# Optimization experiments

Measured on AMD Instinct MI355X. Metric: run time of the kernel, lower is better.

The kernel has to match this reference:

```python
import jax, jax.numpy as jnp
import numpy as np

DIM = 256
HEADS = 8
HEAD_DIM = DIM // HEADS          # 32 (v head dim, also defines scale)
QK_DIM = DIM // HEADS // 2       # 16 (q/k head dim)
SCALE = HEAD_DIM ** -0.5


def conv3x3(x, w, b):
    # x: [B,C,H,W], w: [O,I,3,3] (torch OIHW), padding=1 stride=1 == SAME
    y = jax.lax.conv_general_dilated(
        x, w, window_strides=(1, 1), padding='SAME',
        dimension_numbers=('NCHW', 'OIHW', 'NCHW'))
    return y + b[None, :, None, None]


def setup_inputs() -> dict:
    key = jax.random.key(0)
    ks = jax.random.split(key, 12)
    s = 0.02
    B, C, H, W = 1, DIM, 64, 64
    return {
        'x':       jax.random.normal(ks[0], (B, C, H, W), jnp.float32),
        'attn_kv': jax.random.normal(ks[1], (B, C, H, W), jnp.float32),
        'qw':  jax.random.normal(ks[2], (C, C, 3, 3), jnp.float32) * s,
        'qb':  jnp.zeros((C,), jnp.float32),
        'kvw': jax.random.normal(ks[3], (C, C, 3, 3), jnp.float32) * s,
        'kvb': jnp.zeros((C,), jnp.float32),
        'Wq':  jax.random.normal(ks[4], (C // 2, C), jnp.float32) * s,
        'bq':  jnp.zeros((C // 2,), jnp.float32),
        'Wk':  jax.random.normal(ks[5], (C // 2, C), jnp.float32) * s,
        'bk':  jnp.zeros((C // 2,), jnp.float32),
        'Wv':  jax.random.normal(ks[6], (C, C), jnp.float32) * s,
        'bv':  jnp.zeros((C,), jnp.float32),
        'Wp':  jax.random.normal(ks[7], (C, C), jnp.float32) * s,
        'bp':  jnp.zeros((C,), jnp.float32),
    }


def reference(x, attn_kv, qw, qb, kvw, kvb, Wq, bq, Wk, bk, Wv, bv, Wp, bp):
    B, C, Hh, Ww = x.shape
    N = Hh * Ww
    # conv projections
    xq = conv3x3(x, qw, qb)            # [B,C,H,W]
    kv = conv3x3(attn_kv, kvw, kvb)    # [B,C,H,W]
    # flatten to tokens [B,N,C]
    xf = xq.reshape(B, C, N).transpose(0, 2, 1)
    kvf = kv.reshape(B, C, N).transpose(0, 2, 1)
    # qkv projections with asymmetric head dims
    q = (xf @ Wq.T + bq).reshape(B, N, HEADS, QK_DIM).transpose(0, 2, 1, 3)    # [B,h,N,16]
    k = (kvf @ Wk.T + bk).reshape(B, N, HEADS, QK_DIM).transpose(0, 2, 1, 3)   # [B,h,N,16]
    v = (kvf @ Wv.T + bv).reshape(B, N, HEADS, HEAD_DIM).transpose(0, 2, 1, 3) # [B,h,N,32]
    # attention (manual softmax(q k^T) v)
    attn = jax.nn.softmax(jnp.einsum('bhnd,bhmd->bhnm', q * SCALE, k), axis=-1)  # [B,h,N,N]
    o = jnp.einsum('bhnm,bhmd->bhnd', attn, v)  # [B,h,N,32]
    # replicate the original transpose(1,2).reshape(B,N,C) on the [1,B,h,N,dv]
    # tensor: memory order becomes (h, B, N, dv) flattened into (B, N, C).
    o = jnp.transpose(o, (1, 0, 2, 3)).reshape(B, N, C)
    out = o @ Wp.T + bp                               # [B,N,C]
    return out.transpose(0, 2, 1).reshape(B, C, Hh, Ww)
```

## Files before the change

kernel.cpp:

```cpp
#include <hip/hip_runtime.h>

typedef unsigned short u16;
typedef __attribute__((ext_vector_type(8))) short bf16x8;
typedef __attribute__((ext_vector_type(4))) float f32x4;
typedef __attribute__((ext_vector_type(16))) float f32x16;
typedef __attribute__((ext_vector_type(4))) unsigned u32x4;
typedef __attribute__((ext_vector_type(2))) int i32x2;

struct alignas(8) u16x4 { u16 x, y, z, w; };

#define MFMA16(A, B, C) __builtin_amdgcn_mfma_f32_16x16x32_bf16(A, B, C, 0, 0, 0)
#define MFMA32(A, B, C) __builtin_amdgcn_mfma_f32_32x32x16_bf16(A, B, C, 0, 0, 0)
#define QSCALE (0.17677669529663689f * 1.4426950408889634f)

__device__ __forceinline__ u16 f2bf(float f) {
  unsigned u = __float_as_uint(f);
  u = (u + 0x7fffu + ((u >> 16) & 1u)) >> 16;
  return (u16)u;
}

__device__ __forceinline__ bf16x8 ldb8(const u16* p) {
  return *reinterpret_cast<const bf16x8*>(p);
}

__device__ __forceinline__ void glds16(const u16* g, u16* l) {
  __builtin_amdgcn_global_load_lds(
      (const __attribute__((address_space(1))) void*)g,
      (__attribute__((address_space(3))) void*)l, 16, 0, 0);
}

__global__ __launch_bounds__(256) void prep_kernel(
    const float* __restrict__ x, const float* __restrict__ akv,
    const float* __restrict__ qw, const float* __restrict__ kvw,
    const float* __restrict__ Wq, const float* __restrict__ Wk,
    const float* __restrict__ Wv, const float* __restrict__ Wp,
    u16* __restrict__ xpT, u16* __restrict__ w2,
    u16* __restrict__ wqs, u16* __restrict__ wks,
    u16* __restrict__ wvs, u16* __restrict__ wps)
{
  __shared__ float sm[64 * 65];
  const int b = blockIdx.x, t = threadIdx.x;
  if (b < 512) {
    const int z = b >> 8, rem = b & 255;
    const int cib = (rem >> 6) * 64, y = rem & 63;
    const float* in = (z ? akv : x);
    const int tc = t & 63, tr = t >> 6;
    #pragma unroll
    for (int i = 0; i < 16; ++i) {
      const int ci = i * 4 + tr;
      sm[ci * 65 + tc] = in[(size_t)(cib + ci) * 4096 + y * 64 + tc];
    }
    __syncthreads();
    u16* dst = xpT + (size_t)z * 4356 * 256;
    #pragma unroll
    for (int i = 0; i < 16; ++i) {
      const int px = i * 4 + tr;
      dst[(size_t)((y + 1) * 66 + px + 1) * 256 + cib + tc] = f2bf(sm[tc * 65 + px]);
    }
    return;
  }
  if (b < 642) {
    const int slot = (b - 512) * 4 + (t >> 6);
    const int z = slot >= 260 ? 1 : 0;
    const int j = slot - z * 260;
    int pos;
    if (j < 66) pos = j;
    else if (j < 132) pos = 65 * 66 + (j - 66);
    else { const int j2 = j - 132; pos = (1 + (j2 >> 1)) * 66 + (j2 & 1) * 65; }
    u16x4 zr = {0, 0, 0, 0};
    *reinterpret_cast<u16x4*>(xpT + (size_t)z * 4356 * 256 + (size_t)pos * 256 + (t & 63) * 4) = zr;
    return;
  }
  if (b < 1154) {
    const int idx = b - 642;
    const int z = idx >> 8, co = idx & 255;
    const float* src = (z ? kvw : qw) + (size_t)co * 2304;
    u16* dst = w2 + (size_t)z * 256 * 2304 + (size_t)co * 2304;
    #pragma unroll
    for (int i = 0; i < 9; ++i) sm[i * 256 + t] = src[i * 256 + t];
    __syncthreads();
    #pragma unroll
    for (int i = 0; i < 9; ++i) dst[i * 256 + t] = f2bf(sm[t * 9 + i]);
    return;
  }
  {
    int idx = (b - 1154) * 256 + t;
    if (idx < 32768) { wqs[idx] = f2bf(Wq[idx] * QSCALE); return; }
    idx -= 32768;
    if (idx < 32768) { wks[idx] = f2bf(Wk[idx]); return; }
    idx -= 32768;
    if (idx < 65536) { wvs[idx] = f2bf(Wv[idx]); return; }
    idx -= 65536;
    wps[idx] = f2bf(Wp[idx]);
  }
}

__global__ __launch_bounds__(256, 2) void conv_kernel(
    const u16* __restrict__ xpT, const u16* __restrict__ w2,
    const float* __restrict__ qb, const float* __restrict__ kvb,
    u16* __restrict__ xqt, u16* __restrict__ kvt)
{
  __shared__ u16 ab[3][64 * 64];
  __shared__ u16 bb[3][64 * 64];

  const int z = blockIdx.z;
  const u16* __restrict__ X = xpT + (size_t)z * 4356 * 256;
  const u16* __restrict__ W = w2 + (size_t)z * 256 * 2304;
  const float* bias = z ? kvb : qb;
  u16* out = z ? kvt : xqt;

  const int lane = threadIdx.x & 63, w = threadIdx.x >> 6;
  const int lo = lane & 15, g = lane >> 4;
  const int r8 = lane >> 3, c = lane & 7;
  const int wr = w >> 1, wc = w & 1;
  const int cobase = blockIdx.x * 64;
  const int tbase = blockIdx.y * 64;

  const bool isA = (w < 2);
  const u16* gb[4];
  int ldso[4];
  #pragma unroll
  for (int q = 0; q < 4; ++q) {
    const int flat = w * 4 + q;
    if (flat < 8) {
      const int j = flat;
      gb[q] = W + (size_t)(cobase + j * 8 + r8) * 2304 + (c ^ r8) * 8;
      ldso[q] = j * 512;
    } else {
      const int j = flat - 8;
      const int tok = tbase + j * 8 + r8;
      const int padrow = ((tok >> 6) + 1) * 66 + (tok & 63) + 1;
      gb[q] = X + (size_t)padrow * 256 + (c ^ r8) * 8;
      ldso[q] = j * 512;
    }
  }

  f32x4 acc[2][2] = {};

  auto stage = [&](int s, int bsel) {
    int srcoff;
    if (isA) {
      srcoff = s * 64;
    } else {
      const int kk = s >> 2;
      const int koff = (kk / 3 - 1) * 66 + (kk % 3) - 1;
      srcoff = koff * 256 + (s & 3) * 64;
    }
    u16* lb = isA ? ab[bsel] : bb[bsel];
    #pragma unroll
    for (int q = 0; q < 4; ++q)
      glds16(gb[q] + srcoff, lb + ldso[q]);
  };

  stage(0, 0);
  stage(1, 1);
  asm volatile("s_waitcnt vmcnt(4)" ::: "memory");
  __syncthreads();

  #pragma unroll 1
  for (int s = 0; s < 36; ++s) {
    const int cur = s % 3;
    if (s + 2 < 36) stage(s + 2, (s + 2) % 3);
    #pragma unroll
    for (int ks = 0; ks < 2; ++ks) {
      const int swz = ((ks * 4 + g) ^ (lo & 7)) * 8;
      const int rowA = wr * 32 + lo, colB = wc * 32 + lo;
      bf16x8 a0 = *reinterpret_cast<const bf16x8*>(&ab[cur][rowA * 64 + swz]);
      bf16x8 a1 = *reinterpret_cast<const bf16x8*>(&ab[cur][(rowA + 16) * 64 + swz]);
      bf16x8 b0 = *reinterpret_cast<const bf16x8*>(&bb[cur][colB * 64 + swz]);
      bf16x8 b1 = *reinterpret_cast<const bf16x8*>(&bb[cur][(colB + 16) * 64 + swz]);
      acc[0][0] = MFMA16(a0, b0, acc[0][0]);
      acc[0][1] = MFMA16(a0, b1, acc[0][1]);
      acc[1][0] = MFMA16(a1, b0, acc[1][0]);
      acc[1][1] = MFMA16(a1, b1, acc[1][1]);
    }
    if (s < 35) {
      if (s + 2 < 36) asm volatile("s_waitcnt vmcnt(4)" ::: "memory");
      else            asm volatile("s_waitcnt vmcnt(0)" ::: "memory");
      __syncthreads();
    }
  }

  #pragma unroll
  for (int af = 0; af < 2; ++af) {
    const int cb = cobase + wr * 32 + af * 16 + 4 * g;
    const float4 bi = *reinterpret_cast<const float4*>(bias + cb);
    #pragma unroll
    for (int bf = 0; bf < 2; ++bf) {
      const int t = tbase + wc * 32 + bf * 16 + lo;
      f32x4 v = acc[af][bf];
      u16x4 pk = { f2bf(v[0] + bi.x), f2bf(v[1] + bi.y),
                   f2bf(v[2] + bi.z), f2bf(v[3] + bi.w) };
      *reinterpret_cast<u16x4*>(out + (size_t)t * 256 + cb) = pk;
    }
  }
}

__global__ __launch_bounds__(256) void qkv_kernel(
    const u16* __restrict__ xqt, const u16* __restrict__ kvt,
    const u16* __restrict__ wqs, const u16* __restrict__ wks,
    const u16* __restrict__ wvs,
    const float* __restrict__ bq, const float* __restrict__ bk,
    const float* __restrict__ bv,
    u16* __restrict__ Qh, u16* __restrict__ Kh, u16* __restrict__ Vp)
{
  const int lane = threadIdx.x & 63, wid = threadIdx.x >> 6;
  const int lo = lane & 15, g = lane >> 4;
  const int bx = blockIdx.x;

  if (blockIdx.z == 0) {
    const bool isq = bx < 2;
    const u16* A = isq ? wqs : wks;
    const u16* Bm = isq ? xqt : kvt;
    const float* bias = isq ? bq : bk;
    const float bsc = isq ? (float)QSCALE : 1.f;
    u16* outp = isq ? Qh : Kh;
    const int c0 = (bx & 1) * 64 + (wid >> 1) * 32;
    const int n0 = blockIdx.y * 64 + (wid & 1) * 32;

    f32x4 acc[2][2] = {};
    #pragma unroll
    for (int s = 0; s < 8; ++s) {
      const int k0 = s * 32 + 8 * g;
      bf16x8 A0 = ldb8(A + (c0 + lo) * 256 + k0);
      bf16x8 A1 = ldb8(A + (c0 + 16 + lo) * 256 + k0);
      bf16x8 B0 = ldb8(Bm + (n0 + lo) * 256 + k0);
      bf16x8 B1 = ldb8(Bm + (n0 + 16 + lo) * 256 + k0);
      acc[0][0] = MFMA16(A0, B0, acc[0][0]);
      acc[0][1] = MFMA16(A0, B1, acc[0][1]);
      acc[1][0] = MFMA16(A1, B0, acc[1][0]);
      acc[1][1] = MFMA16(A1, B1, acc[1][1]);
    }
    #pragma unroll
    for (int af = 0; af < 2; ++af) {
      const int cb = c0 + af * 16 + 4 * g;
      const int h = cb >> 4, dd = cb & 15;
      const float4 bi = *reinterpret_cast<const float4*>(bias + cb);
      #pragma unroll
      for (int bfr = 0; bfr < 2; ++bfr) {
        const int n = n0 + bfr * 16 + lo;
        f32x4 v = acc[af][bfr];
        u16x4 pk = { f2bf(v[0] + bi.x * bsc), f2bf(v[1] + bi.y * bsc),
                     f2bf(v[2] + bi.z * bsc), f2bf(v[3] + bi.w * bsc) };
        *reinterpret_cast<u16x4*>(outp + h * 65536 + n * 16 + dd) = pk;
      }
    }
  } else {
    const int n0 = blockIdx.y * 64 + (wid >> 1) * 32;
    const int c0 = bx * 64 + (wid & 1) * 32;

    f32x4 acc[2][2] = {};
    #pragma unroll
    for (int s = 0; s < 8; ++s) {
      const int k0 = s * 32 + 8 * g;
      bf16x8 A0 = ldb8(kvt + (n0 + lo) * 256 + k0);
      bf16x8 A1 = ldb8(kvt + (n0 + 16 + lo) * 256 + k0);
      bf16x8 B0 = ldb8(wvs + (c0 + lo) * 256 + k0);
      bf16x8 B1 = ldb8(wvs + (c0 + 16 + lo) * 256 + k0);
      acc[0][0] = MFMA16(A0, B0, acc[0][0]);
      acc[0][1] = MFMA16(A0, B1, acc[0][1]);
      acc[1][0] = MFMA16(A1, B0, acc[1][0]);
      acc[1][1] = MFMA16(A1, B1, acc[1][1]);
    }
    #pragma unroll
    for (int af = 0; af < 2; ++af) {
      const int nb = n0 + af * 16 + 4 * g;
      const int tblk = nb >> 4, hhalf = (nb >> 3) & 1, j0 = nb & 7;
      #pragma unroll
      for (int bfr = 0; bfr < 2; ++bfr) {
        const int cc = c0 + bfr * 16 + lo;
        const int h = cc >> 5, dv = cc & 31;
        const float bi = bv[cc];
        f32x4 v = acc[af][bfr];
        u16x4 pk = { f2bf(v[0] + bi), f2bf(v[1] + bi),
                     f2bf(v[2] + bi), f2bf(v[3] + bi) };
        *reinterpret_cast<u16x4*>(
            Vp + (size_t)h * 131072 + tblk * 512 + hhalf * 256 + dv * 8 + j0) = pk;
      }
    }
  }
}

__global__ __launch_bounds__(512, 4) void attn_kernel(
    const u16* __restrict__ Qh, const u16* __restrict__ Kh,
    const u16* __restrict__ Vp, u16* __restrict__ O2)
{
  __shared__ float olds[16][8][64];
  __shared__ float l_ldsA[8][32], l_ldsB[8][32];
  __shared__ float invA[32], invB[32];

  const int lane = threadIdx.x & 63, w = threadIdx.x >> 6;
  const int lo = lane & 31, hi = lane >> 5;
  const int bx = blockIdx.x;
  const int h = bx & 7, qg = bx >> 3;
  const int qt0 = qg * 64;

  const u16* Q = Qh + h * 65536;
  const u16* K = Kh + h * 65536;

  const bf16x8 qbA = ldb8(Q + (qt0 + lo) * 16 + 8 * hi);
  const bf16x8 qbB = ldb8(Q + (qt0 + 32 + lo) * 16 + 8 * hi);

  f32x16 oA = {0,0,0,0,0,0,0,0,0,0,0,0,0,0,0,0};
  f32x16 oB = {0,0,0,0,0,0,0,0,0,0,0,0,0,0,0,0};
  float lA0 = 0.f, lA1 = 0.f, lB0 = 0.f, lB1 = 0.f;
  const int kvbase = w * 512;

  const u16* kptr = K + (kvbase + lo) * 16 + 8 * hi;
  const u16* vptr = Vp + (size_t)h * 131072 + (size_t)kvbase * 32 + lane * 8;

  #pragma unroll 1
  for (int st = 0; st < 16; ++st) {
    const bf16x8 kb = ldb8(kptr);
    const bf16x8 vb0 = ldb8(vptr);
    const bf16x8 vb1 = ldb8(vptr + 512);
    kptr += 512; vptr += 1024;

    const f32x16 zf = {0,0,0,0,0,0,0,0,0,0,0,0,0,0,0,0};

    {
      f32x16 s = MFMA32(kb, qbA, zf);
      unsigned cpk[8];
      #pragma unroll
      for (int r = 0; r < 16; r += 2) {
        const float p0 = __builtin_amdgcn_exp2f(s[r]);
        const float p1 = __builtin_amdgcn_exp2f(s[r + 1]);
        lA0 += p0; lA1 += p1;
        asm("v_cvt_pk_bf16_f32 %0, %1, %2" : "=v"(cpk[r >> 1]) : "v"(p0), "v"(p1));
      }
      u32x4 fa0, fa1;
      { i32x2 r2 = __builtin_amdgcn_permlane32_swap((int)cpk[0], (int)cpk[2], false, false);
        fa0[0] = (unsigned)r2[0]; fa0[2] = (unsigned)r2[1]; }
      { i32x2 r2 = __builtin_amdgcn_permlane32_swap((int)cpk[1], (int)cpk[3], false, false);
        fa0[1] = (unsigned)r2[0]; fa0[3] = (unsigned)r2[1]; }
      { i32x2 r2 = __builtin_amdgcn_permlane32_swap((int)cpk[4], (int)cpk[6], false, false);
        fa1[0] = (unsigned)r2[0]; fa1[2] = (unsigned)r2[1]; }
      { i32x2 r2 = __builtin_amdgcn_permlane32_swap((int)cpk[5], (int)cpk[7], false, false);
        fa1[1] = (unsigned)r2[0]; fa1[3] = (unsigned)r2[1]; }
      oA = MFMA32(__builtin_bit_cast(bf16x8, fa0), vb0, oA);
      oA = MFMA32(__builtin_bit_cast(bf16x8, fa1), vb1, oA);
    }
    {
      f32x16 s = MFMA32(kb, qbB, zf);
      unsigned cpk[8];
      #pragma unroll
      for (int r = 0; r < 16; r += 2) {
        const float p0 = __builtin_amdgcn_exp2f(s[r]);
        const float p1 = __builtin_amdgcn_exp2f(s[r + 1]);
        lB0 += p0; lB1 += p1;
        asm("v_cvt_pk_bf16_f32 %0, %1, %2" : "=v"(cpk[r >> 1]) : "v"(p0), "v"(p1));
      }
      u32x4 fa0, fa1;
      { i32x2 r2 = __builtin_amdgcn_permlane32_swap((int)cpk[0], (int)cpk[2], false, false);
        fa0[0] = (unsigned)r2[0]; fa0[2] = (unsigned)r2[1]; }
      { i32x2 r2 = __builtin_amdgcn_permlane32_swap((int)cpk[1], (int)cpk[3], false, false);
        fa0[1] = (unsigned)r2[0]; fa0[3] = (unsigned)r2[1]; }
      { i32x2 r2 = __builtin_amdgcn_permlane32_swap((int)cpk[4], (int)cpk[6], false, false);
        fa1[0] = (unsigned)r2[0]; fa1[2] = (unsigned)r2[1]; }
      { i32x2 r2 = __builtin_amdgcn_permlane32_swap((int)cpk[5], (int)cpk[7], false, false);
        fa1[1] = (unsigned)r2[0]; fa1[3] = (unsigned)r2[1]; }
      oB = MFMA32(__builtin_bit_cast(bf16x8, fa0), vb0, oB);
      oB = MFMA32(__builtin_bit_cast(bf16x8, fa1), vb1, oB);
    }
  }

  float lA = lA0 + lA1;  lA += __shfl_xor(lA, 32);
  float lB = lB0 + lB1;  lB += __shfl_xor(lB, 32);
  if (lane < 32) { l_ldsA[w][lane] = lA; l_ldsB[w][lane] = lB; }

  #pragma unroll
  for (int r = 0; r < 16; ++r) olds[r][w][lane] = oA[r];
  __syncthreads();

  if (w == 0 && lane < 32) {
    float L = 0.f;
    #pragma unroll
    for (int w2 = 0; w2 < 8; ++w2) L += l_ldsA[w2][lane];
    invA[lane] = 1.0f / L;
  }
  if (w == 1 && lane < 32) {
    float L = 0.f;
    #pragma unroll
    for (int w2 = 0; w2 < 8; ++w2) L += l_ldsB[w2][lane];
    invB[lane] = 1.0f / L;
  }
  __syncthreads();

  #pragma unroll
  for (int j = 0; j < 2; ++j) {
    const int r = 2 * w + j;
    const int q = (r & 3) + 8 * (r >> 2) + 4 * hi;
    float acc = 0.f;
    #pragma unroll
    for (int w2 = 0; w2 < 8; ++w2) acc += olds[r][w2][lane];
    acc *= invA[q];
    const int n = qt0 + q;
    O2[(size_t)((h << 9) + (n >> 3)) * 256 + ((n & 7) << 5) + lo] = f2bf(acc);
  }
  __syncthreads();

  #pragma unroll
  for (int r = 0; r < 16; ++r) olds[r][w][lane] = oB[r];
  __syncthreads();

  #pragma unroll
  for (int j = 0; j < 2; ++j) {
    const int r = 2 * w + j;
    const int q = (r & 3) + 8 * (r >> 2) + 4 * hi;
    float acc = 0.f;
    #pragma unroll
    for (int w2 = 0; w2 < 8; ++w2) acc += olds[r][w2][lane];
    acc *= invB[q];
    const int n = qt0 + 32 + q;
    O2[(size_t)((h << 9) + (n >> 3)) * 256 + ((n & 7) << 5) + lo] = f2bf(acc);
  }
}

__global__ __launch_bounds__(256) void oproj_kernel(
    const u16* __restrict__ O2, const u16* __restrict__ wps,
    const float* __restrict__ bp, float* __restrict__ outp)
{
  const int lane = threadIdx.x & 63, wid = threadIdx.x >> 6;
  const int lo = lane & 15, g = lane >> 4;
  const int n0 = blockIdx.x * 64 + (wid >> 1) * 32;
  const int c0 = blockIdx.y * 64 + (wid & 1) * 32;

  f32x4 acc[2][2] = {};
  #pragma unroll
  for (int s = 0; s < 8; ++s) {
    const int k0 = s * 32 + 8 * g;
    bf16x8 A0 = ldb8(O2 + (n0 + lo) * 256 + k0);
    bf16x8 A1 = ldb8(O2 + (n0 + 16 + lo) * 256 + k0);
    bf16x8 B0 = ldb8(wps + (c0 + lo) * 256 + k0);
    bf16x8 B1 = ldb8(wps + (c0 + 16 + lo) * 256 + k0);
    acc[0][0] = MFMA16(A0, B0, acc[0][0]);
    acc[0][1] = MFMA16(A0, B1, acc[0][1]);
    acc[1][0] = MFMA16(A1, B0, acc[1][0]);
    acc[1][1] = MFMA16(A1, B1, acc[1][1]);
  }
  #pragma unroll
  for (int af = 0; af < 2; ++af) {
    const int nb = n0 + af * 16 + 4 * g;
    #pragma unroll
    for (int bfr = 0; bfr < 2; ++bfr) {
      const int c = c0 + bfr * 16 + lo;
      const float bi = bp[c];
      f32x4 v = acc[af][bfr];
      float4 r4;
      r4.x = v[0] + bi; r4.y = v[1] + bi; r4.z = v[2] + bi; r4.w = v[3] + bi;
      *reinterpret_cast<float4*>(outp + (size_t)c * 4096 + nb) = r4;
    }
  }
}

extern "C" void kernel_launch(void* const* d_in, const int* in_sizes, int n_in,
                              void* d_out, int out_size, void* d_ws, size_t ws_size,
                              hipStream_t stream) {
  (void)in_sizes; (void)n_in; (void)out_size; (void)ws_size;
  const float* x   = (const float*)d_in[0];
  const float* akv = (const float*)d_in[1];
  const float* qw  = (const float*)d_in[2];
  const float* qb  = (const float*)d_in[3];
  const float* kvw = (const float*)d_in[4];
  const float* kvb = (const float*)d_in[5];
  const float* Wq  = (const float*)d_in[6];
  const float* bq  = (const float*)d_in[7];
  const float* Wk  = (const float*)d_in[8];
  const float* bk  = (const float*)d_in[9];
  const float* Wv  = (const float*)d_in[10];
  const float* bv  = (const float*)d_in[11];
  const float* Wp  = (const float*)d_in[12];
  const float* bp  = (const float*)d_in[13];
  float* outp = (float*)d_out;

  char* wsb = (char*)d_ws;
  size_t off = 0;
  auto take = [&](size_t bytes) {
    char* p = wsb + off;
    off = (off + bytes + 255) & ~(size_t)255;
    return p;
  };
  u16* xpT = (u16*)take(2ULL * 4356 * 256 * 2);
  u16* w2  = (u16*)take(2ULL * 256 * 2304 * 2);
  u16* wqs = (u16*)take(128ULL * 256 * 2);
  u16* wks = (u16*)take(128ULL * 256 * 2);
  u16* wvs = (u16*)take(256ULL * 256 * 2);
  u16* wps = (u16*)take(256ULL * 256 * 2);
  u16* xqt = (u16*)take(4096ULL * 256 * 2);
  u16* kvt = (u16*)take(4096ULL * 256 * 2);
  u16* Qh  = (u16*)take(8ULL * 4096 * 16 * 2);
  u16* Kh  = (u16*)take(8ULL * 4096 * 16 * 2);
  u16* Vp  = (u16*)take(8ULL * 131072 * 2);
  u16* O2  = (u16*)take(4096ULL * 256 * 2);

  prep_kernel<<<dim3(1922), dim3(256), 0, stream>>>(
      x, akv, qw, kvw, Wq, Wk, Wv, Wp, xpT, w2, wqs, wks, wvs, wps);
  conv_kernel<<<dim3(4, 64, 2), dim3(256), 0, stream>>>(xpT, w2, qb, kvb, xqt, kvt);
  qkv_kernel<<<dim3(4, 64, 2), dim3(256), 0, stream>>>(
      xqt, kvt, wqs, wks, wvs, bq, bk, bv, Qh, Kh, Vp);
  attn_kernel<<<dim3(512), dim3(512), 0, stream>>>(Qh, Kh, Vp, O2);
  oproj_kernel<<<dim3(64, 4), dim3(256), 0, stream>>>(O2, wps, bp, outp);
}
```

Baseline: 70.05 us.

## Software-prefetch operands in qkv/attn loops and shrink oproj tiles for more blocks

Adds register double-buffering to the qkv, attention and output-projection inner loops, loading the next K-step's operands before issuing the current MFMAs so global load latency overlaps with compute. The attention loop also issues both score MFMAs up front. The output projection is retiled from 32x32 per wave to 16x16 per wave with four times as many blocks, which raises parallelism but loses operand reuse. The extra live registers could reduce occupancy.

```diff
diff --git a/kernel.cpp b/kernel.cpp
--- a/kernel.cpp
+++ b/kernel.cpp
@@ -218,18 +218,26 @@
     const int c0 = (bx & 1) * 64 + (wid >> 1) * 32;
     const int n0 = blockIdx.y * 64 + (wid & 1) * 32;
 
+    const u16* Ar0 = A + (c0 + lo) * 256 + 8 * g;
+    const u16* Ar1 = A + (c0 + 16 + lo) * 256 + 8 * g;
+    const u16* Br0 = Bm + (n0 + lo) * 256 + 8 * g;
+    const u16* Br1 = Bm + (n0 + 16 + lo) * 256 + 8 * g;
+
     f32x4 acc[2][2] = {};
+    bf16x8 A0 = ldb8(Ar0), A1 = ldb8(Ar1), B0 = ldb8(Br0), B1 = ldb8(Br1);
     #pragma unroll
     for (int s = 0; s < 8; ++s) {
-      const int k0 = s * 32 + 8 * g;
-      bf16x8 A0 = ldb8(A + (c0 + lo) * 256 + k0);
-      bf16x8 A1 = ldb8(A + (c0 + 16 + lo) * 256 + k0);
-      bf16x8 B0 = ldb8(Bm + (n0 + lo) * 256 + k0);
-      bf16x8 B1 = ldb8(Bm + (n0 + 16 + lo) * 256 + k0);
+      bf16x8 A0n, A1n, B0n, B1n;
+      if (s < 7) {
+        const int kn = (s + 1) * 32;
+        A0n = ldb8(Ar0 + kn); A1n = ldb8(Ar1 + kn);
+        B0n = ldb8(Br0 + kn); B1n = ldb8(Br1 + kn);
+      }
       acc[0][0] = MFMA16(A0, B0, acc[0][0]);
       acc[0][1] = MFMA16(A0, B1, acc[0][1]);
       acc[1][0] = MFMA16(A1, B0, acc[1][0]);
       acc[1][1] = MFMA16(A1, B1, acc[1][1]);
+      A0 = A0n; A1 = A1n; B0 = B0n; B1 = B1n;
     }
     #pragma unroll
     for (int af = 0; af < 2; ++af) {
@@ -249,18 +257,26 @@
     const int n0 = blockIdx.y * 64 + (wid >> 1) * 32;
     const int c0 = bx * 64 + (wid & 1) * 32;
 
+    const u16* Ar0 = kvt + (n0 + lo) * 256 + 8 * g;
+    const u16* Ar1 = kvt + (n0 + 16 + lo) * 256 + 8 * g;
+    const u16* Br0 = wvs + (c0 + lo) * 256 + 8 * g;
+    const u16* Br1 = wvs + (c0 + 16 + lo) * 256 + 8 * g;
+
     f32x4 acc[2][2] = {};
+    bf16x8 A0 = ldb8(Ar0), A1 = ldb8(Ar1), B0 = ldb8(Br0), B1 = ldb8(Br1);
     #pragma unroll
     for (int s = 0; s < 8; ++s) {
-      const int k0 = s * 32 + 8 * g;
-      bf16x8 A0 = ldb8(kvt + (n0 + lo) * 256 + k0);
-      bf16x8 A1 = ldb8(kvt + (n0 + 16 + lo) * 256 + k0);
-      bf16x8 B0 = ldb8(wvs + (c0 + lo) * 256 + k0);
-      bf16x8 B1 = ldb8(wvs + (c0 + 16 + lo) * 256 + k0);
+      bf16x8 A0n, A1n, B0n, B1n;
+      if (s < 7) {
+        const int kn = (s + 1) * 32;
+        A0n = ldb8(Ar0 + kn); A1n = ldb8(Ar1 + kn);
+        B0n = ldb8(Br0 + kn); B1n = ldb8(Br1 + kn);
+      }
       acc[0][0] = MFMA16(A0, B0, acc[0][0]);
       acc[0][1] = MFMA16(A0, B1, acc[0][1]);
       acc[1][0] = MFMA16(A1, B0, acc[1][0]);
       acc[1][1] = MFMA16(A1, B1, acc[1][1]);
+      A0 = A0n; A1 = A1n; B0 = B0n; B1 = B1n;
     }
     #pragma unroll
     for (int af = 0; af < 2; ++af) {
@@ -309,22 +325,27 @@
   const u16* kptr = K + (kvbase + lo) * 16 + 8 * hi;
   const u16* vptr = Vp + (size_t)h * 131072 + (size_t)kvbase * 32 + lane * 8;
 
+  bf16x8 kb = ldb8(kptr);
+  bf16x8 vb0 = ldb8(vptr);
+  bf16x8 vb1 = ldb8(vptr + 512);
+
   #pragma unroll 1
   for (int st = 0; st < 16; ++st) {
-    const bf16x8 kb = ldb8(kptr);
-    const bf16x8 vb0 = ldb8(vptr);
-    const bf16x8 vb1 = ldb8(vptr + 512);
     kptr += 512; vptr += 1024;
+    const bf16x8 kb_n = ldb8(kptr);
+    const bf16x8 vb0_n = ldb8(vptr);
+    const bf16x8 vb1_n = ldb8(vptr + 512);
 
     const f32x16 zf = {0,0,0,0,0,0,0,0,0,0,0,0,0,0,0,0};
+    f32x16 sA = MFMA32(kb, qbA, zf);
+    f32x16 sB = MFMA32(kb, qbB, zf);
 
     {
-      f32x16 s = MFMA32(kb, qbA, zf);
       unsigned cpk[8];
       #pragma unroll
       for (int r = 0; r < 16; r += 2) {
-        const float p0 = __builtin_amdgcn_exp2f(s[r]);
-        const float p1 = __builtin_amdgcn_exp2f(s[r + 1]);
+        const float p0 = __builtin_amdgcn_exp2f(sA[r]);
+        const float p1 = __builtin_amdgcn_exp2f(sA[r + 1]);
         lA0 += p0; lA1 += p1;
         asm("v_cvt_pk_bf16_f32 %0, %1, %2" : "=v"(cpk[r >> 1]) : "v"(p0), "v"(p1));
       }
@@ -341,12 +362,11 @@
       oA = MFMA32(__builtin_bit_cast(bf16x8, fa1), vb1, oA);
     }
     {
-      f32x16 s = MFMA32(kb, qbB, zf);
       unsigned cpk[8];
       #pragma unroll
       for (int r = 0; r < 16; r += 2) {
-        const float p0 = __builtin_amdgcn_exp2f(s[r]);
-        const float p1 = __builtin_amdgcn_exp2f(s[r + 1]);
+        const float p0 = __builtin_amdgcn_exp2f(sB[r]);
+        const float p1 = __builtin_amdgcn_exp2f(sB[r + 1]);
         lB0 += p0; lB1 += p1;
         asm("v_cvt_pk_bf16_f32 %0, %1, %2" : "=v"(cpk[r >> 1]) : "v"(p0), "v"(p1));
       }
@@ -362,6 +382,7 @@
       oB = MFMA32(__builtin_bit_cast(bf16x8, fa0), vb0, oB);
       oB = MFMA32(__builtin_bit_cast(bf16x8, fa1), vb1, oB);
     }
+    kb = kb_n; vb0 = vb0_n; vb1 = vb1_n;
   }
 
   float lA = lA0 + lA1;  lA += __shfl_xor(lA, 32);
@@ -422,35 +443,29 @@
 {
   const int lane = threadIdx.x & 63, wid = threadIdx.x >> 6;
   const int lo = lane & 15, g = lane >> 4;
-  const int n0 = blockIdx.x * 64 + (wid >> 1) * 32;
-  const int c0 = blockIdx.y * 64 + (wid & 1) * 32;
-
-  f32x4 acc[2][2] = {};
+  const int n0 = blockIdx.x * 16;
+  const int c0 = blockIdx.y * 64 + wid * 16;
+
+  const u16* Ar = O2 + (n0 + lo) * 256 + 8 * g;
+  const u16* Br = wps + (c0 + lo) * 256 + 8 * g;
+
+  f32x4 acc = {};
+  bf16x8 A0 = ldb8(Ar), B0 = ldb8(Br);
   #pragma unroll
   for (int s = 0; s < 8; ++s) {
-    const int k0 = s * 32 + 8 * g;
-    bf16x8 A0 = ldb8(O2 + (n0 + lo) * 256 + k0);
-    bf16x8 A1 = ldb8(O2 + (n0 + 16 + lo) * 256 + k0);
-    bf16x8 B0 = ldb8(wps + (c0 + lo) * 256 + k0);
-    bf16x8 B1 = ldb8(wps + (c0 + 16 + lo) * 256 + k0);
-    acc[0][0] = MFMA16(A0, B0, acc[0][0]);
-    acc[0][1] = MFMA16(A0, B1, acc[0][1]);
-    acc[1][0] = MFMA16(A1, B0, acc[1][0]);
-    acc[1][1] = MFMA16(A1, B1, acc[1][1]);
-  }
-  #pragma unroll
-  for (int af = 0; af < 2; ++af) {
-    const int nb = n0 + af * 16 + 4 * g;
-    #pragma unroll
-    for (int bfr = 0; bfr < 2; ++bfr) {
-      const int c = c0 + bfr * 16 + lo;
-      const float bi = bp[c];
-      f32x4 v = acc[af][bfr];
-      float4 r4;
-      r4.x = v[0] + bi; r4.y = v[1] + bi; r4.z = v[2] + bi; r4.w = v[3] + bi;
-      *reinterpret_cast<float4*>(outp + (size_t)c * 4096 + nb) = r4;
-    }
-  }
+    bf16x8 A0n, B0n;
+    if (s < 7) {
+      const int kn = (s + 1) * 32;
+      A0n = ldb8(Ar + kn); B0n = ldb8(Br + kn);
+    }
+    acc = MFMA16(A0, B0, acc);
+    A0 = A0n; B0 = B0n;
+  }
+  const int c = c0 + lo;
+  const float bi = bp[c];
+  float4 r4;
+  r4.x = acc[0] + bi; r4.y = acc[1] + bi; r4.z = acc[2] + bi; r4.w = acc[3] + bi;
+  *reinterpret_cast<float4*>(outp + (size_t)c * 4096 + n0 + 4 * g) = r4;
 }
 
 extern "C" void kernel_launch(void* const* d_in, const int* in_sizes, int n_in,
@@ -499,5 +514,5 @@
   qkv_kernel<<<dim3(4, 64, 2), dim3(256), 0, stream>>>(
       xqt, kvt, wqs, wks, wvs, bq, bk, bv, Qh, Kh, Vp);
   attn_kernel<<<dim3(512), dim3(512), 0, stream>>>(Qh, Kh, Vp, O2);
-  oproj_kernel<<<dim3(64, 4), dim3(256), 0, stream>>>(O2, wps, bp, outp);
-}
+  oproj_kernel<<<dim3(256, 4), dim3(256), 0, stream>>>(O2, wps, bp, outp);
+}
```

Result: slower. 73.46 us (+4.9%).
